# Optimization experiments

Measured on AMD Instinct MI355X. Metric: run time of the kernel, lower is better.

Reference implementation:

```python
import jax, jax.numpy as jnp
import numpy as np

TOP_K = 2


def setup_inputs() -> dict:
    key = jax.random.key(0)
    ks = jax.random.split(key, 8)
    B, S, D, E = 4, 2048, 768, 8
    F = 4 * D
    scale = 0.02
    x = jax.random.normal(ks[0], (B, S, D), dtype=jnp.float32)
    router_w = jax.random.normal(ks[1], (D, E), dtype=jnp.float32) * scale
    router_b = jnp.zeros((E,), dtype=jnp.float32)
    w1 = jax.random.normal(ks[2], (E, D, F), dtype=jnp.float32) * scale
    b1 = jnp.zeros((E, F), dtype=jnp.float32)
    w2 = jax.random.normal(ks[3], (E, F, D), dtype=jnp.float32) * scale
    b2 = jnp.zeros((E, D), dtype=jnp.float32)
    return {"x": x, "router_w": router_w, "router_b": router_b,
            "w1": w1, "b1": b1, "w2": w2, "b2": b2}


def reference(x, router_w, router_b, w1, b1, w2, b2):
    E = w1.shape[0]
    # router: [B,S,E]
    logits = jnp.einsum('bsd,de->bse', x, router_w) + router_b
    probs = jax.nn.softmax(logits, axis=-1)
    top_p, top_i = jax.lax.top_k(probs, TOP_K)          # [B,S,K]
    top_p = top_p / jnp.sum(top_p, axis=-1, keepdims=True)
    # dense combine weights [B,S,E]: renormalized top-k prob if selected else 0
    combine = jnp.sum(jax.nn.one_hot(top_i, E, dtype=x.dtype) * top_p[..., None], axis=-2)
    # loop over small fixed expert count (structurally distinct weight slices)
    out = jnp.zeros_like(x)
    for e in range(E):
        h = jax.nn.gelu(jnp.einsum('bsd,df->bsf', x, w1[e]) + b1[e], approximate=False)
        y = jnp.einsum('bsf,fd->bsd', h, w2[e]) + b2[e]
        out = out + combine[..., e:e + 1] * y
    return out
```

## Files before the change

### kernel.cpp

```cpp
#include <hip/hip_runtime.h>
#include <hip/hip_bf16.h>
#include <math.h>

#define TOKENS 8192
#define Dm 768
#define Fm 3072
#define Em 8
#define BM 256
#define BN 256
#define BK 64

typedef __attribute__((ext_vector_type(8))) short short8v;
typedef __attribute__((ext_vector_type(4))) short short4v;
typedef __attribute__((ext_vector_type(4))) float f32x4;

__device__ inline short f2b(float f) {
  __hip_bfloat16 h = __float2bfloat16(f);
  return *reinterpret_cast<short*>(&h);
}

__device__ inline void async16(short* lds, const short* g) {
  __builtin_amdgcn_global_load_lds((const __attribute__((address_space(1))) void*)g,
                                   (__attribute__((address_space(3))) void*)lds, 16, 0, 0);
}

__global__ __launch_bounds__(256) void cvt_tr_kernel(const float* __restrict__ in,
                                                     short* __restrict__ out, int R, int C) {
  __shared__ short tile[64][68];
  size_t eoff = (size_t)blockIdx.z * R * C;
  const float* inp = in + eoff;
  short* outp = out + eoff;
  int tc = blockIdx.x * 64, tr = blockIdx.y * 64;
  {
    int row = threadIdx.x >> 2;
    int cch = (threadIdx.x & 3) * 16;
    const float* src = inp + (size_t)(tr + row) * C + tc + cch;
    #pragma unroll
    for (int q = 0; q < 4; q++) {
      float4 v = *(const float4*)(src + q * 4);
      tile[row][cch + q * 4 + 0] = f2b(v.x);
      tile[row][cch + q * 4 + 1] = f2b(v.y);
      tile[row][cch + q * 4 + 2] = f2b(v.z);
      tile[row][cch + q * 4 + 3] = f2b(v.w);
    }
  }
  __syncthreads();
  {
    int c = threadIdx.x >> 2;
    int rch = (threadIdx.x & 3) * 16;
    short tmp[16];
    #pragma unroll
    for (int i = 0; i < 16; i++) tmp[i] = tile[rch + i][c];
    short* dst = outp + (size_t)(tc + c) * R + tr + rch;
    *(short8v*)(dst) = *(short8v*)(tmp);
    *(short8v*)(dst + 8) = *(short8v*)(tmp + 8);
  }
}

__global__ __launch_bounds__(256) void router_kernel(
    const float* __restrict__ x, const float* __restrict__ rw,
    const float* __restrict__ rb, short* __restrict__ xb,
    int2* __restrict__ meta_e, float2* __restrict__ meta_p) {
  int wave = threadIdx.x >> 6;
  int lane = threadIdx.x & 63;
  int t = blockIdx.x * 4 + wave;
  if (t >= TOKENS) return;
  const float* xr = x + (size_t)t * Dm;
  short* xbr = xb + (size_t)t * Dm;
  float acc[Em];
  #pragma unroll
  for (int e = 0; e < Em; e++) acc[e] = 0.f;
  #pragma unroll
  for (int i = 0; i < 3; i++) {
    int d = i * 256 + lane * 4;
    float4 v = *(const float4*)(xr + d);
    short4v s;
    s[0] = f2b(v.x); s[1] = f2b(v.y); s[2] = f2b(v.z); s[3] = f2b(v.w);
    *(short4v*)(xbr + d) = s;
    #pragma unroll
    for (int j = 0; j < 4; j++) {
      float xv = (j == 0) ? v.x : (j == 1) ? v.y : (j == 2) ? v.z : v.w;
      const float4* rwp = (const float4*)(rw + (size_t)(d + j) * Em);
      float4 a = rwp[0], b = rwp[1];
      acc[0] += xv * a.x; acc[1] += xv * a.y; acc[2] += xv * a.z; acc[3] += xv * a.w;
      acc[4] += xv * b.x; acc[5] += xv * b.y; acc[6] += xv * b.z; acc[7] += xv * b.w;
    }
  }
  #pragma unroll
  for (int e = 0; e < Em; e++) {
    float v = acc[e];
    #pragma unroll
    for (int s = 32; s > 0; s >>= 1) v += __shfl_xor(v, s);
    acc[e] = v + rb[e];
  }
  int i1 = 0; float m1 = acc[0];
  #pragma unroll
  for (int e = 1; e < Em; e++) if (acc[e] > m1) { m1 = acc[e]; i1 = e; }
  int i2 = -1; float m2 = -1e30f;
  #pragma unroll
  for (int e = 0; e < Em; e++) if (e != i1 && acc[e] > m2) { m2 = acc[e]; i2 = e; }
  float tt = expf(m2 - m1);
  float p0 = 1.f / (1.f + tt);
  float p1 = tt / (1.f + tt);
  if (lane == 0) {
    meta_e[t] = make_int2(i1, i2);
    meta_p[t] = make_float2(p0, p1);
  }
}

__global__ __launch_bounds__(256) void scatter_kernel(
    const int2* __restrict__ meta_e, int* __restrict__ cnt,
    int* __restrict__ list, int4* __restrict__ meta_i) {
  __shared__ int lcnt[Em];
  __shared__ int gbase[Em];
  int t = blockIdx.x * 256 + threadIdx.x;
  if (threadIdx.x < Em) lcnt[threadIdx.x] = 0;
  __syncthreads();
  int2 e = meta_e[t];
  int r0 = atomicAdd(&lcnt[e.x], 1);
  int r1 = atomicAdd(&lcnt[e.y], 1);
  __syncthreads();
  if (threadIdx.x < Em) gbase[threadIdx.x] = atomicAdd(&cnt[threadIdx.x], lcnt[threadIdx.x]);
  __syncthreads();
  int s0 = gbase[e.x] + r0;
  int s1 = gbase[e.y] + r1;
  list[e.x * TOKENS + s0] = t;
  list[e.y * TOKENS + s1] = t;
  meta_i[t] = make_int4(e.x, s0, e.y, s1);
}

__global__ void prefix_kernel(const int* __restrict__ cnt, int* __restrict__ hoffs) {
  if (threadIdx.x == 0) {
    int s = 0;
    for (int e = 0; e < Em; e++) { hoffs[e] = s; s += cnt[e]; }
  }
}

template <int MODE>
__global__ __launch_bounds__(512, 2) void moe_gemm_kernel(
    const short* __restrict__ Abase, const short* __restrict__ Wt,
    const float* __restrict__ bias, short* __restrict__ Hout,
    float* __restrict__ Yout, const int* __restrict__ cnt,
    const int* __restrict__ hoffs, const int* __restrict__ list,
    int Ndim, int Kdim) {
  int e = blockIdx.z;
  int count = cnt[e];
  int mbase = blockIdx.y * BM;
  if (mbase >= count) return;
  int n0 = blockIdx.x * BN;
  int ho = hoffs[e];

  __shared__ short As[2 * BM * BK];
  __shared__ short Bs[2 * BN * BK];
  __shared__ int rid_s[BM];

  int tid = threadIdx.x;
  if (MODE == 0) {
    if (tid < BM) {
      int rc = mbase + tid; if (rc > count - 1) rc = count - 1;
      rid_s[tid] = list[e * TOKENS + rc];
    }
  }
  __syncthreads();

  const short* We = Wt + (size_t)e * Ndim * Kdim;
  int swz = ((tid & 7) ^ ((tid >> 3) & 7)) * 8;
  const short* aptr[4];
  const short* bptr[4];
  #pragma unroll
  for (int q = 0; q < 4; q++) {
    int rloc = q * 64 + (tid >> 3);
    size_t grow;
    if (MODE == 0) {
      grow = (size_t)rid_s[rloc] * Kdim;
    } else {
      int rr = mbase + rloc; if (rr > count - 1) rr = count - 1;
      grow = (size_t)(ho + rr) * Kdim;
    }
    aptr[q] = Abase + grow + swz;
    bptr[q] = We + (size_t)(n0 + rloc) * Kdim + swz;
  }
  int w = tid >> 6;

  #define STAGE(s)                                              \
    {                                                           \
      _Pragma("unroll")                                         \
      for (int q = 0; q < 4; q++) {                             \
        async16(&As[(s) * (BM * BK) + q * 4096 + w * 512], aptr[q]); \
        async16(&Bs[(s) * (BN * BK) + q * 4096 + w * 512], bptr[q]); \
        aptr[q] += BK; bptr[q] += BK;                           \
      }                                                         \
    }

  int NT = Kdim / BK;
  STAGE(0);
  STAGE(1);
  asm volatile("s_waitcnt vmcnt(8)" ::: "memory");
  __builtin_amdgcn_s_barrier();

  f32x4 acc[8][4] = {};
  int lane = tid & 63;
  int wm = (tid >> 6) >> 2, wn = (tid >> 6) & 3;
  int lr = lane & 15, lh = lane >> 4;
  int rsw = lr & 7;

  for (int t = 0; t < NT; t++) {
    int s = t & 1;
    const short* Ab = &As[s * (BM * BK)];
    const short* Bb = &Bs[s * (BN * BK)];
    short8v a0[8], b0[4];
    #pragma unroll
    for (int m = 0; m < 8; m++)
      a0[m] = *(const short8v*)&Ab[(wm * 128 + m * 16 + lr) * 64 + ((lh ^ rsw) * 8)];
    #pragma unroll
    for (int n = 0; n < 4; n++)
      b0[n] = *(const short8v*)&Bb[(wn * 64 + n * 16 + lr) * 64 + ((lh ^ rsw) * 8)];
    __builtin_amdgcn_s_setprio(1);
    #pragma unroll
    for (int m = 0; m < 8; m++)
      #pragma unroll
      for (int n = 0; n < 4; n++)
        acc[m][n] = __builtin_amdgcn_mfma_f32_16x16x32_bf16(a0[m], b0[n], acc[m][n], 0, 0, 0);
    __builtin_amdgcn_s_setprio(0);
    short8v a1[8], b1v[4];
    #pragma unroll
    for (int m = 0; m < 8; m++)
      a1[m] = *(const short8v*)&Ab[(wm * 128 + m * 16 + lr) * 64 + (((4 + lh) ^ rsw) * 8)];
    #pragma unroll
    for (int n = 0; n < 4; n++)
      b1v[n] = *(const short8v*)&Bb[(wn * 64 + n * 16 + lr) * 64 + (((4 + lh) ^ rsw) * 8)];
    asm volatile("s_waitcnt lgkmcnt(0)" ::: "memory");
    __builtin_amdgcn_sched_barrier(0);
    __builtin_amdgcn_s_barrier();
    if (t + 2 < NT) STAGE(s);
    __builtin_amdgcn_s_setprio(1);
    #pragma unroll
    for (int m = 0; m < 8; m++)
      #pragma unroll
      for (int n = 0; n < 4; n++)
        acc[m][n] = __builtin_amdgcn_mfma_f32_16x16x32_bf16(a1[m], b1v[n], acc[m][n], 0, 0, 0);
    __builtin_amdgcn_s_setprio(0);
    if (t + 2 < NT)
      asm volatile("s_waitcnt vmcnt(8)" ::: "memory");
    else
      asm volatile("s_waitcnt vmcnt(0)" ::: "memory");
    __builtin_amdgcn_s_barrier();
  }

  if (MODE == 0) {
    const float* be = bias + (size_t)e * Ndim;
    #pragma unroll
    for (int m = 0; m < 8; m++) {
      #pragma unroll
      for (int j = 0; j < 4; j++) {
        int r = wm * 128 + m * 16 + lh * 4 + j;
        if (mbase + r < count) {
          size_t rowoff = (size_t)(ho + mbase + r) * Ndim;
          #pragma unroll
          for (int n = 0; n < 4; n++) {
            int colg = n0 + wn * 64 + n * 16 + lr;
            float val = acc[m][n][j] + be[colg];
            float z = val * 0.70710678118654752f;
            float az = fabsf(z);
            float tt = __fdividef(1.f, fmaf(0.3275911f, az, 1.f));
            float poly = fmaf(fmaf(fmaf(fmaf(1.061405429f, tt, -1.453152027f), tt,
                              1.421413741f), tt, -0.284496736f), tt, 0.254829592f) * tt;
            float er = 1.f - poly * __expf(-az * az);
            er = z < 0.f ? -er : er;
            val = 0.5f * val * (1.f + er);
            Hout[rowoff + colg] = f2b(val);
          }
        }
      }
    }
  } else {
    #pragma unroll
    for (int m = 0; m < 8; m++) {
      #pragma unroll
      for (int j = 0; j < 4; j++) {
        int r = wm * 128 + m * 16 + lh * 4 + j;
        if (mbase + r < count) {
          float* yrow = Yout + (size_t)(ho + mbase + r) * Ndim;
          #pragma unroll
          for (int n = 0; n < 4; n++) {
            int colg = n0 + wn * 64 + n * 16 + lr;
            yrow[colg] = acc[m][n][j];
          }
        }
      }
    }
  }
  #undef STAGE
}

__global__ __launch_bounds__(256) void combine_kernel(
    const float* __restrict__ Y, const float* __restrict__ b2,
    const int* __restrict__ hoffs, const int4* __restrict__ meta_i,
    const float2* __restrict__ meta_p, float* __restrict__ out) {
  int wave = threadIdx.x >> 6;
  int lane = threadIdx.x & 63;
  int t = blockIdx.x * 4 + wave;
  if (t >= TOKENS) return;
  int4 mi = meta_i[t];
  float2 mp = meta_p[t];
  const float4* y0 = (const float4*)(Y + (size_t)(hoffs[mi.x] + mi.y) * Dm);
  const float4* y1 = (const float4*)(Y + (size_t)(hoffs[mi.z] + mi.w) * Dm);
  const float4* ba = (const float4*)(b2 + (size_t)mi.x * Dm);
  const float4* bb = (const float4*)(b2 + (size_t)mi.z * Dm);
  float4* orow = (float4*)(out + (size_t)t * Dm);
  #pragma unroll
  for (int i = 0; i < 3; i++) {
    int idx = lane + 64 * i;
    float4 v0 = y0[idx], v1 = y1[idx], a = ba[idx], b = bb[idx];
    float4 o;
    o.x = mp.x * (v0.x + a.x) + mp.y * (v1.x + b.x);
    o.y = mp.x * (v0.y + a.y) + mp.y * (v1.y + b.y);
    o.z = mp.x * (v0.z + a.z) + mp.y * (v1.z + b.z);
    o.w = mp.x * (v0.w + a.w) + mp.y * (v1.w + b.w);
    orow[idx] = o;
  }
}

extern "C" void kernel_launch(void* const* d_in, const int* in_sizes, int n_in,
                              void* d_out, int out_size, void* d_ws, size_t ws_size,
                              hipStream_t stream) {
  const float* x  = (const float*)d_in[0];
  const float* rw = (const float*)d_in[1];
  const float* rb = (const float*)d_in[2];
  const float* w1 = (const float*)d_in[3];
  const float* b1 = (const float*)d_in[4];
  const float* w2 = (const float*)d_in[5];
  const float* b2 = (const float*)d_in[6];
  float* out = (float*)d_out;
  char* ws = (char*)d_ws;

  const size_t off_cnt    = 0;
  const size_t off_hoffs  = 64;
  const size_t off_list   = 1024;
  const size_t off_meta_i = off_list + (size_t)Em * TOKENS * 4;
  const size_t off_meta_p = off_meta_i + (size_t)TOKENS * 16;
  const size_t off_meta_e = off_meta_p + (size_t)TOKENS * 8;
  const size_t off_xbf    = off_meta_e + (size_t)TOKENS * 8;
  const size_t off_w1t    = off_xbf + (size_t)TOKENS * Dm * 2;
  const size_t off_w2t    = off_w1t + (size_t)Em * Dm * Fm * 2;
  const size_t off_h      = off_w2t + (size_t)Em * Fm * Dm * 2;
  const size_t needed     = off_h + (size_t)2 * TOKENS * Fm * 2;
  if (ws_size < needed) return;

  int*    cnt    = (int*)(ws + off_cnt);
  int*    hoffs  = (int*)(ws + off_hoffs);
  int*    list   = (int*)(ws + off_list);
  int4*   meta_i = (int4*)(ws + off_meta_i);
  float2* meta_p = (float2*)(ws + off_meta_p);
  int2*   meta_e = (int2*)(ws + off_meta_e);
  short*  xbf    = (short*)(ws + off_xbf);
  short*  w1t    = (short*)(ws + off_w1t);
  short*  w2t    = (short*)(ws + off_w2t);
  short*  h      = (short*)(ws + off_h);
  float*  y      = (float*)(ws + off_xbf);

  hipMemsetAsync(cnt, 0, 32, stream);
  cvt_tr_kernel<<<dim3(Fm / 64, Dm / 64, Em), 256, 0, stream>>>(w1, w1t, Dm, Fm);
  cvt_tr_kernel<<<dim3(Dm / 64, Fm / 64, Em), 256, 0, stream>>>(w2, w2t, Fm, Dm);
  router_kernel<<<TOKENS / 4, 256, 0, stream>>>(x, rw, rb, xbf, meta_e, meta_p);
  scatter_kernel<<<TOKENS / 256, 256, 0, stream>>>(meta_e, cnt, list, meta_i);
  prefix_kernel<<<1, 64, 0, stream>>>(cnt, hoffs);
  moe_gemm_kernel<0><<<dim3(Fm / BN, TOKENS / BM, Em), 512, 0, stream>>>(
      xbf, w1t, b1, h, nullptr, cnt, hoffs, list, Fm, Dm);
  moe_gemm_kernel<1><<<dim3(Dm / BN, TOKENS / BM, Em), 512, 0, stream>>>(
      h, w2t, nullptr, nullptr, y, cnt, hoffs, list, Dm, Fm);
  combine_kernel<<<TOKENS / 4, 256, 0, stream>>>(y, b2, hoffs, meta_i, meta_p, out);
}
```

Before: 337.1 us.

## Use compact tile table with 128x128 single-buffered MoE GEMM tiles

Replaces the dense expert-by-m-block grid, where most blocks exit early, with a tile table built in the prefix kernel that lists only valid (expert, m-block) pairs. The block tile shrinks from 256x256 with 512 threads and double-buffered async LDS loads to 128x128 with 256 threads, a single LDS buffer and plain __syncthreads. The goal is fewer wasted blocks, more blocks for the small N=768 second GEMM, and higher occupancy. The cost is losing the load/compute overlap from double buffering and lower arithmetic intensity per tile.

After: 364.0 us. +8.0%, slower.

```diff
diff --git a/kernel.cpp b/kernel.cpp
--- a/kernel.cpp
+++ b/kernel.cpp
@@ -6,8 +6,6 @@
 #define Dm 768
 #define Fm 3072
 #define Em 8
-#define BM 256
-#define BN 256
 #define BK 64
 
 typedef __attribute__((ext_vector_type(8))) short short8v;
@@ -129,34 +127,42 @@
   meta_i[t] = make_int4(e.x, s0, e.y, s1);
 }
 
-__global__ void prefix_kernel(const int* __restrict__ cnt, int* __restrict__ hoffs) {
+__global__ void prefix_kernel(const int* __restrict__ cnt, int* __restrict__ hoffs,
+                              int2* __restrict__ table, int* __restrict__ ntab) {
   if (threadIdx.x == 0) {
-    int s = 0;
-    for (int e = 0; e < Em; e++) { hoffs[e] = s; s += cnt[e]; }
+    int s = 0, k = 0;
+    for (int e = 0; e < Em; e++) {
+      hoffs[e] = s;
+      int c = cnt[e];
+      for (int mb = 0; mb < c; mb += 128) table[k++] = make_int2(e, mb);
+      s += c;
+    }
+    ntab[0] = k;
   }
 }
 
 template <int MODE>
-__global__ __launch_bounds__(512, 2) void moe_gemm_kernel(
+__global__ __launch_bounds__(256, 3) void moe_gemm_kernel(
     const short* __restrict__ Abase, const short* __restrict__ Wt,
     const float* __restrict__ bias, short* __restrict__ Hout,
     float* __restrict__ Yout, const int* __restrict__ cnt,
     const int* __restrict__ hoffs, const int* __restrict__ list,
+    const int2* __restrict__ table, const int* __restrict__ ntab,
     int Ndim, int Kdim) {
-  int e = blockIdx.z;
-  int count = cnt[e];
-  int mbase = blockIdx.y * BM;
-  if (mbase >= count) return;
-  int n0 = blockIdx.x * BN;
-  int ho = hoffs[e];
-
-  __shared__ short As[2 * BM * BK];
-  __shared__ short Bs[2 * BN * BK];
-  __shared__ int rid_s[BM];
+  int ti = blockIdx.y;
+  if (ti >= ntab[0]) return;
+  int2 te = table[ti];
+  int e = te.x, mbase = te.y;
+  int count = cnt[e], ho = hoffs[e];
+  int n0 = blockIdx.x * 128;
+
+  __shared__ short As[128 * 64];
+  __shared__ short Bs[128 * 64];
+  __shared__ int rid_s[128];
 
   int tid = threadIdx.x;
   if (MODE == 0) {
-    if (tid < BM) {
+    if (tid < 128) {
       int rc = mbase + tid; if (rc > count - 1) rc = count - 1;
       rid_s[tid] = list[e * TOKENS + rc];
     }
@@ -164,96 +170,63 @@
   __syncthreads();
 
   const short* We = Wt + (size_t)e * Ndim * Kdim;
-  int swz = ((tid & 7) ^ ((tid >> 3) & 7)) * 8;
   const short* aptr[4];
   const short* bptr[4];
   #pragma unroll
   for (int q = 0; q < 4; q++) {
-    int rloc = q * 64 + (tid >> 3);
+    int r = q * 32 + (tid >> 3);
+    int g = (tid & 7) ^ (r & 7);
     size_t grow;
     if (MODE == 0) {
-      grow = (size_t)rid_s[rloc] * Kdim;
+      grow = (size_t)rid_s[r] * Kdim;
     } else {
-      int rr = mbase + rloc; if (rr > count - 1) rr = count - 1;
+      int rr = mbase + r; if (rr > count - 1) rr = count - 1;
       grow = (size_t)(ho + rr) * Kdim;
     }
-    aptr[q] = Abase + grow + swz;
-    bptr[q] = We + (size_t)(n0 + rloc) * Kdim + swz;
+    aptr[q] = Abase + grow + g * 8;
+    bptr[q] = We + (size_t)(n0 + r) * Kdim + g * 8;
   }
   int w = tid >> 6;
-
-  #define STAGE(s)                                              \
-    {                                                           \
-      _Pragma("unroll")                                         \
-      for (int q = 0; q < 4; q++) {                             \
-        async16(&As[(s) * (BM * BK) + q * 4096 + w * 512], aptr[q]); \
-        async16(&Bs[(s) * (BN * BK) + q * 4096 + w * 512], bptr[q]); \
-        aptr[q] += BK; bptr[q] += BK;                           \
-      }                                                         \
-    }
-
   int NT = Kdim / BK;
-  STAGE(0);
-  STAGE(1);
-  asm volatile("s_waitcnt vmcnt(8)" ::: "memory");
-  __builtin_amdgcn_s_barrier();
-
-  f32x4 acc[8][4] = {};
+
+  f32x4 acc[4][4] = {};
   int lane = tid & 63;
-  int wm = (tid >> 6) >> 2, wn = (tid >> 6) & 3;
+  int wm = w >> 1, wn = w & 1;
   int lr = lane & 15, lh = lane >> 4;
   int rsw = lr & 7;
 
   for (int t = 0; t < NT; t++) {
-    int s = t & 1;
-    const short* Ab = &As[s * (BM * BK)];
-    const short* Bb = &Bs[s * (BN * BK)];
-    short8v a0[8], b0[4];
-    #pragma unroll
-    for (int m = 0; m < 8; m++)
-      a0[m] = *(const short8v*)&Ab[(wm * 128 + m * 16 + lr) * 64 + ((lh ^ rsw) * 8)];
-    #pragma unroll
-    for (int n = 0; n < 4; n++)
-      b0[n] = *(const short8v*)&Bb[(wn * 64 + n * 16 + lr) * 64 + ((lh ^ rsw) * 8)];
-    __builtin_amdgcn_s_setprio(1);
-    #pragma unroll
-    for (int m = 0; m < 8; m++)
+    #pragma unroll
+    for (int q = 0; q < 4; q++) {
+      async16(&As[q * 2048 + w * 512], aptr[q]); aptr[q] += BK;
+      async16(&Bs[q * 2048 + w * 512], bptr[q]); bptr[q] += BK;
+    }
+    __syncthreads();
+    #pragma unroll
+    for (int kk = 0; kk < 2; kk++) {
+      short8v a[4], b[4];
+      #pragma unroll
+      for (int m = 0; m < 4; m++)
+        a[m] = *(const short8v*)&As[(wm * 64 + m * 16 + lr) * 64 + ((kk * 4 + lh) ^ rsw) * 8];
       #pragma unroll
       for (int n = 0; n < 4; n++)
-        acc[m][n] = __builtin_amdgcn_mfma_f32_16x16x32_bf16(a0[m], b0[n], acc[m][n], 0, 0, 0);
-    __builtin_amdgcn_s_setprio(0);
-    short8v a1[8], b1v[4];
-    #pragma unroll
-    for (int m = 0; m < 8; m++)
-      a1[m] = *(const short8v*)&Ab[(wm * 128 + m * 16 + lr) * 64 + (((4 + lh) ^ rsw) * 8)];
-    #pragma unroll
-    for (int n = 0; n < 4; n++)
-      b1v[n] = *(const short8v*)&Bb[(wn * 64 + n * 16 + lr) * 64 + (((4 + lh) ^ rsw) * 8)];
-    asm volatile("s_waitcnt lgkmcnt(0)" ::: "memory");
-    __builtin_amdgcn_sched_barrier(0);
-    __builtin_amdgcn_s_barrier();
-    if (t + 2 < NT) STAGE(s);
-    __builtin_amdgcn_s_setprio(1);
-    #pragma unroll
-    for (int m = 0; m < 8; m++)
-      #pragma unroll
-      for (int n = 0; n < 4; n++)
-        acc[m][n] = __builtin_amdgcn_mfma_f32_16x16x32_bf16(a1[m], b1v[n], acc[m][n], 0, 0, 0);
-    __builtin_amdgcn_s_setprio(0);
-    if (t + 2 < NT)
-      asm volatile("s_waitcnt vmcnt(8)" ::: "memory");
-    else
-      asm volatile("s_waitcnt vmcnt(0)" ::: "memory");
-    __builtin_amdgcn_s_barrier();
+        b[n] = *(const short8v*)&Bs[(wn * 64 + n * 16 + lr) * 64 + ((kk * 4 + lh) ^ rsw) * 8];
+      #pragma unroll
+      for (int m = 0; m < 4; m++)
+        #pragma unroll
+        for (int n = 0; n < 4; n++)
+          acc[m][n] = __builtin_amdgcn_mfma_f32_16x16x32_bf16(a[m], b[n], acc[m][n], 0, 0, 0);
+    }
+    __syncthreads();
   }
 
   if (MODE == 0) {
     const float* be = bias + (size_t)e * Ndim;
     #pragma unroll
-    for (int m = 0; m < 8; m++) {
+    for (int m = 0; m < 4; m++) {
       #pragma unroll
       for (int j = 0; j < 4; j++) {
-        int r = wm * 128 + m * 16 + lh * 4 + j;
+        int r = wm * 64 + m * 16 + lh * 4 + j;
         if (mbase + r < count) {
           size_t rowoff = (size_t)(ho + mbase + r) * Ndim;
           #pragma unroll
@@ -275,10 +248,10 @@
     }
   } else {
     #pragma unroll
-    for (int m = 0; m < 8; m++) {
+    for (int m = 0; m < 4; m++) {
       #pragma unroll
       for (int j = 0; j < 4; j++) {
-        int r = wm * 128 + m * 16 + lh * 4 + j;
+        int r = wm * 64 + m * 16 + lh * 4 + j;
         if (mbase + r < count) {
           float* yrow = Yout + (size_t)(ho + mbase + r) * Ndim;
           #pragma unroll
@@ -290,7 +263,6 @@
       }
     }
   }
-  #undef STAGE
 }
 
 __global__ __launch_bounds__(256) void combine_kernel(
@@ -336,7 +308,9 @@
 
   const size_t off_cnt    = 0;
   const size_t off_hoffs  = 64;
-  const size_t off_list   = 1024;
+  const size_t off_ntab   = 128;
+  const size_t off_table  = 192;
+  const size_t off_list   = 2048;
   const size_t off_meta_i = off_list + (size_t)Em * TOKENS * 4;
   const size_t off_meta_p = off_meta_i + (size_t)TOKENS * 16;
   const size_t off_meta_e = off_meta_p + (size_t)TOKENS * 8;
@@ -349,6 +323,8 @@
 
   int*    cnt    = (int*)(ws + off_cnt);
   int*    hoffs  = (int*)(ws + off_hoffs);
+  int*    ntab   = (int*)(ws + off_ntab);
+  int2*   table  = (int2*)(ws + off_table);
   int*    list   = (int*)(ws + off_list);
   int4*   meta_i = (int4*)(ws + off_meta_i);
   float2* meta_p = (float2*)(ws + off_meta_p);
@@ -364,10 +340,10 @@
   cvt_tr_kernel<<<dim3(Dm / 64, Fm / 64, Em), 256, 0, stream>>>(w2, w2t, Fm, Dm);
   router_kernel<<<TOKENS / 4, 256, 0, stream>>>(x, rw, rb, xbf, meta_e, meta_p);
   scatter_kernel<<<TOKENS / 256, 256, 0, stream>>>(meta_e, cnt, list, meta_i);
-  prefix_kernel<<<1, 64, 0, stream>>>(cnt, hoffs);
-  moe_gemm_kernel<0><<<dim3(Fm / BN, TOKENS / BM, Em), 512, 0, stream>>>(
-      xbf, w1t, b1, h, nullptr, cnt, hoffs, list, Fm, Dm);
-  moe_gemm_kernel<1><<<dim3(Dm / BN, TOKENS / BM, Em), 512, 0, stream>>>(
-      h, w2t, nullptr, nullptr, y, cnt, hoffs, list, Dm, Fm);
+  prefix_kernel<<<1, 64, 0, stream>>>(cnt, hoffs, table, ntab);
+  moe_gemm_kernel<0><<<dim3(Fm / 128, 136), 256, 0, stream>>>(
+      xbf, w1t, b1, h, nullptr, cnt, hoffs, list, table, ntab, Fm, Dm);
+  moe_gemm_kernel<1><<<dim3(Dm / 128, 136), 256, 0, stream>>>(
+      h, w2t, nullptr, nullptr, y, cnt, hoffs, list, table, ntab, Dm, Fm);
   combine_kernel<<<TOKENS / 4, 256, 0, stream>>>(y, b2, hoffs, meta_i, meta_p, out);
 }
```
